# Kernel tuning notes

Measured on AMD Instinct MI355X. Metric: run time of the kernel, lower is better.

The kernel has to match this reference:

```python
import jax, jax.numpy as jnp
import numpy as np

NUM_HEADS = 32
NUM_FEATURES = 512
CPH = NUM_FEATURES // NUM_HEADS  # 16


def _grouped_1x1(x_flat, w, b, groups):
    # x_flat: (B, Cin); w: (Cout, Cin//groups); b: (Cout,)
    B, Cin = x_flat.shape
    Cout = w.shape[0]
    xg = x_flat.reshape(B, groups, Cin // groups)
    wg = w.reshape(groups, Cout // groups, Cin // groups)
    out = jnp.einsum('bgi,goi->bgo', xg, wg).reshape(B, Cout) + b
    return out


def _attend(x, w, b):
    # x: (B, C, H, W, Z) zero-mean input; w: (num_heads, CPH); b: (num_heads,)
    B, C, H, W, Z = x.shape
    N = H * W * Z
    xr = x.reshape(B, NUM_HEADS, CPH, N)
    # grouped 1x1 conv producing one attention logit map per head
    logits = jnp.einsum('bhcn,hc->bhn', xr, w) + b[None, :, None]
    attn = jax.nn.softmax(logits, axis=-1)  # softmax over spatial
    res = jnp.einsum('bhcn,bhn->bhc', xr, attn)  # weighted pooling
    return res.reshape(B, C, 1, 1, 1)


def setup_inputs() -> dict:
    key = jax.random.key(0)
    ks = jax.random.split(key, 7)
    C = NUM_FEATURES
    x = jax.random.normal(ks[0], (4, C, 32, 32, 32), dtype=jnp.float32)
    # P module: conv1 C->C/2 groups=32, conv2 C/2->C groups=32 (kaiming-like scale)
    pw1 = jax.random.normal(ks[1], (C // 2, C // NUM_HEADS), dtype=jnp.float32) * np.float32(np.sqrt(2.0 / (C // 2)))
    pb1 = jnp.zeros((C // 2,), dtype=jnp.float32)
    pw2 = jax.random.normal(ks[2], (C, (C // 2) // NUM_HEADS), dtype=jnp.float32) * np.float32(np.sqrt(2.0 / C))
    pb2 = jnp.zeros((C,), dtype=jnp.float32)
    kw = jax.random.normal(ks[3], (NUM_HEADS, CPH), dtype=jnp.float32) * np.float32(np.sqrt(2.0 / NUM_HEADS))
    kb = jnp.zeros((NUM_HEADS,), dtype=jnp.float32)
    qw = jax.random.normal(ks[4], (NUM_HEADS, CPH), dtype=jnp.float32) * np.float32(np.sqrt(2.0 / NUM_HEADS))
    qb = jnp.zeros((NUM_HEADS,), dtype=jnp.float32)
    return {"x": x, "pw1": pw1, "pb1": pb1, "pw2": pw2, "pb2": pb2,
            "kw": kw, "kb": kb, "qw": qw, "qb": qb}


def reference(x, pw1, pb1, pw2, pb2, kw, kb, qw, qb):
    B, C, H, W, Z = x.shape
    mu = x.mean(axis=(2, 3, 4), keepdims=True)  # (B,C,1,1,1)
    x_mu = x - mu
    # P: grouped bottleneck MLP on mu with sigmoid gate
    h1 = jax.nn.relu(_grouped_1x1(mu.reshape(B, C), pw1, pb1, NUM_HEADS))
    P = jax.nn.sigmoid(_grouped_1x1(h1, pw2, pb2, NUM_HEADS)).reshape(B, C, 1, 1, 1)
    K = _attend(x_mu, kw, kb)
    Q = _attend(x_mu, qw, qb)
    y = (x + K - Q) * P
    dp = jnp.mean(K * Q, axis=1, keepdims=True)  # (B,1,1,1,1)
    return (y, dp)
```

## Files before the change

### kernel.cpp

```cpp
#include <hip/hip_runtime.h>
#include <math.h>

namespace {

constexpr int B = 4;
constexpr int C = 512;
constexpr int NH = 32;
constexpr int CPH = 16;
constexpr int N = 32 * 32 * 32;
constexpr int MST = 512;
constexpr int NST = 4;
constexpr int NJB = 16;
constexpr int NREC = NJB * 4;
constexpr long YSIZE = (long)B * C * N;

typedef float f4v __attribute__((ext_vector_type(4)));

__device__ inline float wrs(float v) {
#pragma unroll
  for (int o = 32; o > 0; o >>= 1) v += __shfl_xor(v, o);
  return v;
}

template <int CTRL, int RM = 0xF>
__device__ __forceinline__ float dppAdd(float v) {
  const int r = __builtin_amdgcn_update_dpp(
      0, __float_as_int(v), CTRL, RM, 0xF, true);
  return v + __int_as_float(r);
}
__device__ __forceinline__ float waveSumRow3(float v) {
  v = dppAdd<0xB1>(v);
  v = dppAdd<0x4E>(v);
  v = dppAdd<0x124>(v);
  v = dppAdd<0x128>(v);
  v = dppAdd<0x142, 0xA>(v);
  v = dppAdd<0x143, 0xC>(v);
  return v;
}

__global__ __launch_bounds__(256, 2) void kA(const float* __restrict__ x,
                                             const float* __restrict__ kw,
                                             const float* __restrict__ qw,
                                             float* __restrict__ prec) {
  const int b = blockIdx.z, h = blockIdx.y, j = blockIdx.x;
  const int t = threadIdx.x, lane = t & 63, wid = t >> 6;
  const int p = lane & 15;
  const float* xh = x + ((long)(b * C + h * CPH)) * N + (long)j * (NST * MST);

  __shared__ float lds[2][CPH][MST];

  float wk[CPH], wq[CPH];
#pragma unroll
  for (int c = 0; c < CPH; ++c) {
    wk[c] = kw[h * CPH + c];
    wq[c] = qw[h * CPH + c];
  }

  float dk[CPH], dq[CPH], cs[CPH];
#pragma unroll
  for (int c = 0; c < CPH; ++c) { dk[c] = 0.f; dq[c] = 0.f; cs[c] = 0.f; }
  float sK = 0.f, sQ = 0.f;

  auto stage = [&](int s, int buf) {
    const float* src = xh + (long)s * MST;
#pragma unroll
    for (int i = 0; i < 4; ++i) {
      const int c = wid * 4 + i;
#pragma unroll
      for (int k = 0; k < 2; ++k) {
        const float4 v = *(const float4*)(src + (long)c * N + k * 256 + lane * 4);
        *(float4*)&lds[buf][c][k * 256 + lane * 4] = v;
      }
    }
  };

  auto compute = [&](int buf) {
#pragma unroll
    for (int nn = 0; nn < 2; ++nn) {
      const int n = nn * 256 + t;
      float xv[CPH];
#pragma unroll
      for (int c = 0; c < CPH; ++c) xv[c] = lds[buf][c][n];
      float lk = 0.f, lq = 0.f;
#pragma unroll
      for (int c = 0; c < CPH; ++c) { lk += xv[c] * wk[c]; lq += xv[c] * wq[c]; }
      const float ek = __expf(lk), eq = __expf(lq);
      sK += ek; sQ += eq;
#pragma unroll
      for (int c = 0; c < CPH; ++c) {
        dk[c] += xv[c] * ek;
        dq[c] += xv[c] * eq;
        cs[c] += xv[c];
      }
    }
  };

  stage(0, 0);
  __syncthreads();
#pragma unroll
  for (int s = 0; s < NST; ++s) {
    if (s + 1 < NST) stage(s + 1, (s + 1) & 1);
    compute(s & 1);
    __syncthreads();
  }

  const float tsK = waveSumRow3(sK);
  const float tsQ = waveSumRow3(sQ);
  float o0 = 0.f, o1 = 0.f, o2 = 0.f;
#pragma unroll
  for (int c = 0; c < CPH; ++c) {
    const float rk = waveSumRow3(dk[c]);
    const float rq = waveSumRow3(dq[c]);
    const float rc = waveSumRow3(cs[c]);
    if (p == c) { o0 = rk; o1 = rq; o2 = rc; }
  }
  const float o3 = (p == 0) ? tsK : ((p == 1) ? tsQ : 0.f);

  if ((lane >> 4) == 3) {
    const long ridx = (((long)(b * NH + h)) * NJB + j) * 4 + wid;
    f4v r; r.x = o0; r.y = o1; r.z = o2; r.w = o3;
    *(f4v*)(prec + ridx * 64 + p * 4) = r;
  }
}

__global__ __launch_bounds__(512) void k4(const float* __restrict__ prec,
                                          const float* __restrict__ pw1,
                                          const float* __restrict__ pb1,
                                          const float* __restrict__ pw2,
                                          const float* __restrict__ pb2,
                                          float* __restrict__ scale,
                                          float* __restrict__ offset,
                                          float* __restrict__ dpOut) {
  const int b = blockIdx.x;
  const int c = threadIdx.x;
  const int h = c >> 4, i = c & 15;
  const float4* rec4 = (const float4*)prec + ((long)(b * NH + h)) * NREC * 16;

  float dk = 0.f, dq = 0.f, cs = 0.f, sacc = 0.f;
  for (int j = 0; j < NREC; ++j) {
    const float4 r = rec4[j * 16 + i];
    dk += r.x; dq += r.y; cs += r.z; sacc += r.w;
  }
  __shared__ float skS[NH], sqS[NH];
  if (i == 0) skS[h] = sacc;
  if (i == 1) sqS[h] = sacc;
  __syncthreads();
  const float sk = skS[h], sq = sqS[h];

  const float mu = cs * (1.f / N);
  const float Kv = dk / sk - mu;
  const float Qv = dq / sq - mu;

  __shared__ float muS[C], h1S[256];
  muS[c] = mu;
  __syncthreads();
  if (c < 256) {
    const int g = c >> 3;
    float a = pb1[c];
#pragma unroll
    for (int k = 0; k < 16; ++k) a += muS[g * 16 + k] * pw1[c * 16 + k];
    h1S[c] = fmaxf(a, 0.f);
  }
  __syncthreads();
  float a = pb2[c];
  const int g2 = c >> 4;
#pragma unroll
  for (int k = 0; k < 8; ++k) a += h1S[g2 * 8 + k] * pw2[c * 8 + k];
  const float P = 1.f / (1.f + __expf(-a));
  scale[b * C + c] = P;
  offset[b * C + c] = (Kv - Qv) * P;

  float pdp = wrs(Kv * Qv);
  __shared__ float pS[8];
  const int lane = c & 63, wid = c >> 6;
  if (lane == 0) pS[wid] = pdp;
  __syncthreads();
  if (c == 0) {
    float tot = 0.f;
    for (int w = 0; w < 8; ++w) tot += pS[w];
    dpOut[b] = tot * (1.f / C);
  }
}

__global__ __launch_bounds__(256) void k5(const float* __restrict__ x,
                                          const float* __restrict__ scale,
                                          const float* __restrict__ offset,
                                          float* __restrict__ y) {
  const int b = blockIdx.z, cc = blockIdx.y;
  const int t = threadIdx.x;
  const long base = ((long)(b * C + cc)) * N + (long)blockIdx.x * 4096;
  const float s = scale[b * C + cc], o = offset[b * C + cc];
#pragma unroll
  for (int k = 0; k < 4; ++k) {
    const long i = base + (long)(k * 256 + t) * 4;
    const f4v v = __builtin_nontemporal_load((const f4v*)(x + i));
    f4v w;
    w.x = v.x * s + o; w.y = v.y * s + o;
    w.z = v.z * s + o; w.w = v.w * s + o;
    __builtin_nontemporal_store(w, (f4v*)(y + i));
  }
}

}

extern "C" void kernel_launch(void* const* d_in, const int* in_sizes, int n_in,
                              void* d_out, int out_size, void* d_ws, size_t ws_size,
                              hipStream_t stream) {
  const float* x   = (const float*)d_in[0];
  const float* pw1 = (const float*)d_in[1];
  const float* pb1 = (const float*)d_in[2];
  const float* pw2 = (const float*)d_in[3];
  const float* pb2 = (const float*)d_in[4];
  const float* kw  = (const float*)d_in[5];
  const float* qw  = (const float*)d_in[7];
  float* out = (float*)d_out;
  float* ws  = (float*)d_ws;

  float* scale  = ws;
  float* offset = ws + 2048;

  constexpr long PREC = (long)B * NH * NREC * 64;
  float* prec;
  if (ws_size >= (size_t)(4096 + PREC) * sizeof(float)) {
    prec = ws + 4096;
  } else {
    prec = out;
  }

  hipLaunchKernelGGL(kA, dim3(NJB, NH, B), dim3(256), 0, stream,
                     x, kw, qw, prec);
  hipLaunchKernelGGL(k4, dim3(B), dim3(C), 0, stream,
                     prec, pw1, pb1, pw2, pb2, scale, offset, out + YSIZE);
  hipLaunchKernelGGL(k5, dim3(N / 4096, C, B), dim3(256), 0, stream,
                     x, scale, offset, out);
}
```

Baseline: 139.1 us.

## Use direct global-to-LDS loads with triple-buffered two-stage prefetch in kA

Replaces the register-staged float4 copy into LDS with global_load_lds instructions that write straight into shared memory. The buffering goes from two to three buffers and prefetches two stages ahead, with explicit vmcnt waits and barriers. Stage size is halved and occupancy hint raised to 3 blocks per CU. The aim is to drop the VGPR round trip and hide more HBM latency in this memory-bound reduction, at the cost of hand-written waitcnt logic that must match the number of outstanding loads.

Result: no change. 138.3 us (-0.6%).

```diff
diff --git a/kernel.cpp b/kernel.cpp
--- a/kernel.cpp
+++ b/kernel.cpp
@@ -8,8 +8,8 @@
 constexpr int NH = 32;
 constexpr int CPH = 16;
 constexpr int N = 32 * 32 * 32;
-constexpr int MST = 512;
-constexpr int NST = 4;
+constexpr int MST = 256;
+constexpr int NST = 8;
 constexpr int NJB = 16;
 constexpr int NREC = NJB * 4;
 constexpr long YSIZE = (long)B * C * N;
@@ -38,7 +38,7 @@
   return v;
 }
 
-__global__ __launch_bounds__(256, 2) void kA(const float* __restrict__ x,
+__global__ __launch_bounds__(256, 3) void kA(const float* __restrict__ x,
                                              const float* __restrict__ kw,
                                              const float* __restrict__ qw,
                                              float* __restrict__ prec) {
@@ -47,7 +47,7 @@
   const int p = lane & 15;
   const float* xh = x + ((long)(b * C + h * CPH)) * N + (long)j * (NST * MST);
 
-  __shared__ float lds[2][CPH][MST];
+  __shared__ float lds[3][CPH][MST];
 
   float wk[CPH], wq[CPH];
 #pragma unroll
@@ -61,47 +61,48 @@
   for (int c = 0; c < CPH; ++c) { dk[c] = 0.f; dq[c] = 0.f; cs[c] = 0.f; }
   float sK = 0.f, sQ = 0.f;
 
-  auto stage = [&](int s, int buf) {
-    const float* src = xh + (long)s * MST;
+  auto stage = [&](int s) {
+    const int buf = s % 3;
 #pragma unroll
     for (int i = 0; i < 4; ++i) {
       const int c = wid * 4 + i;
-#pragma unroll
-      for (int k = 0; k < 2; ++k) {
-        const float4 v = *(const float4*)(src + (long)c * N + k * 256 + lane * 4);
-        *(float4*)&lds[buf][c][k * 256 + lane * 4] = v;
-      }
+      const float* g = xh + (long)s * MST + (long)c * N + lane * 4;
+      __builtin_amdgcn_global_load_lds(
+          (const __attribute__((address_space(1))) unsigned int*)g,
+          (__attribute__((address_space(3))) unsigned int*)&lds[buf][c][0],
+          16, 0, 0);
     }
   };
 
   auto compute = [&](int buf) {
-#pragma unroll
-    for (int nn = 0; nn < 2; ++nn) {
-      const int n = nn * 256 + t;
-      float xv[CPH];
-#pragma unroll
-      for (int c = 0; c < CPH; ++c) xv[c] = lds[buf][c][n];
-      float lk = 0.f, lq = 0.f;
-#pragma unroll
-      for (int c = 0; c < CPH; ++c) { lk += xv[c] * wk[c]; lq += xv[c] * wq[c]; }
-      const float ek = __expf(lk), eq = __expf(lq);
-      sK += ek; sQ += eq;
-#pragma unroll
-      for (int c = 0; c < CPH; ++c) {
-        dk[c] += xv[c] * ek;
-        dq[c] += xv[c] * eq;
-        cs[c] += xv[c];
-      }
+    float xv[CPH];
+#pragma unroll
+    for (int c = 0; c < CPH; ++c) xv[c] = lds[buf][c][t];
+    float lk = 0.f, lq = 0.f;
+#pragma unroll
+    for (int c = 0; c < CPH; ++c) { lk += xv[c] * wk[c]; lq += xv[c] * wq[c]; }
+    const float ek = __expf(lk), eq = __expf(lq);
+    sK += ek; sQ += eq;
+#pragma unroll
+    for (int c = 0; c < CPH; ++c) {
+      dk[c] += xv[c] * ek;
+      dq[c] += xv[c] * eq;
+      cs[c] += xv[c];
     }
   };
 
-  stage(0, 0);
-  __syncthreads();
+  stage(0);
+  stage(1);
 #pragma unroll
   for (int s = 0; s < NST; ++s) {
-    if (s + 1 < NST) stage(s + 1, (s + 1) & 1);
-    compute(s & 1);
-    __syncthreads();
+    if (s + 2 < NST) stage(s + 2);
+    if (s + 2 < NST)      asm volatile("s_waitcnt vmcnt(8)" ::: "memory");
+    else if (s + 1 < NST) asm volatile("s_waitcnt vmcnt(4)" ::: "memory");
+    else                  asm volatile("s_waitcnt vmcnt(0)" ::: "memory");
+    __builtin_amdgcn_s_barrier();
+    compute(s % 3);
+    asm volatile("" ::: "memory");
+    __builtin_amdgcn_s_barrier();
   }
 
   const float tsK = waveSumRow3(sK);
```
